# Kernel optimization log

Hardware: AMD Instinct MI355X
Metric: run time of the kernel (lower is better)

## Reference

```python
import jax, jax.numpy as jnp
import numpy as np
import math

B, T, C, H = 4, 2048, 1024, 16
D = C // H  # head dim = 64


def setup_inputs() -> dict:
    key = jax.random.key(0)
    ks = jax.random.split(key, 5)
    scale = 0.02
    x = jax.random.normal(ks[0], (B, T, C), dtype=jnp.float32)
    # torch nn.Linear(n_embd, 3*n_embd): weight [3C, C]; we store transposed [C, 3C]
    W_kqv = jax.random.normal(ks[1], (C, 3 * C), dtype=jnp.float32) * scale
    b_kqv = jnp.zeros((3 * C,), dtype=jnp.float32)
    W_proj = jax.random.normal(ks[2], (C, C), dtype=jnp.float32) * scale
    b_proj = jnp.zeros((C,), dtype=jnp.float32)
    padding_mask = jnp.ones((B, T), dtype=jnp.int32)  # 1 = valid token
    return {"x": x, "W_kqv": W_kqv, "b_kqv": b_kqv, "W_proj": W_proj,
            "b_proj": b_proj, "padding_mask": padding_mask}


def reference(x, W_kqv, b_kqv, W_proj, b_proj, padding_mask):
    Bx, Tx, Cx = x.shape
    kqv = x @ W_kqv + b_kqv                      # [B,T,3C]
    # original splits as k, q, v (in that order)
    k, q, v = jnp.split(kqv, 3, axis=2)
    def heads(t):
        return t.reshape(Bx, Tx, H, D).transpose(0, 2, 1, 3)  # [B,H,T,D]
    k, q, v = heads(k), heads(q), heads(v)
    att = jnp.einsum('bhqd,bhkd->bhqk', q, k) * (1.0 / math.sqrt(D))  # [B,H,T,T]
    causal = jnp.tril(jnp.ones((Tx, Tx), dtype=bool))[None, None]     # [1,1,T,T]
    valid = causal & (padding_mask[:, None, None, :] != 0)            # [B,1,T,T] broadcast
    neg_inf = jnp.finfo(att.dtype).min
    att = jnp.where(valid, att, neg_inf)
    att = jax.nn.softmax(att, axis=-1)
    y = jnp.einsum('bhqk,bhkd->bhqd', att, v)    # [B,H,T,D]
    y = y.transpose(0, 2, 1, 3).reshape(Bx, Tx, Cx)
    return y @ W_proj + b_proj
```

## Files before the change

### kernel.cpp

```cpp
#include <hip/hip_runtime.h>


typedef short bf16x8 __attribute__((ext_vector_type(8)));
typedef float floatx4 __attribute__((ext_vector_type(4)));

#define MFMA16(a, b, c) __builtin_amdgcn_mfma_f32_16x16x32_bf16(a, b, c, 0, 0, 0)

#define ASYNC_COPY16(gp, lp)                                                   \
  __builtin_amdgcn_global_load_lds(                                            \
      (__attribute__((address_space(1))) void*)(gp),                           \
      (__attribute__((address_space(3))) void*)(lp), 16, 0, 0)

#define DRAIN_VMCNT() asm volatile("s_waitcnt vmcnt(0)" ::: "memory")

#if defined(__has_builtin)
#if __has_builtin(__builtin_amdgcn_exp2f)
#define EXP2(x) __builtin_amdgcn_exp2f(x)
#endif
#endif
#ifndef EXP2
#define EXP2(x) exp2f(x)
#endif

__device__ __forceinline__ short f2bf(float f) {
  union { float f; unsigned u; } c;
  c.f = f;
  unsigned r = c.u + 0x7fffu + ((c.u >> 16) & 1u);
  return (short)(r >> 16);
}

__global__ __launch_bounds__(256) void cvt_f32_bf16(const float* __restrict__ in,
                                                    short* __restrict__ out) {
  int i = (blockIdx.x * 256 + threadIdx.x) * 4;
  float4 v = *(const float4*)&in[i];
  short4 o;
  o.x = f2bf(v.x); o.y = f2bf(v.y); o.z = f2bf(v.z); o.w = f2bf(v.w);
  *(short4*)&out[i] = o;
}

__global__ __launch_bounds__(256) void pmb_kernel(const int* __restrict__ pm,
                                                  float* __restrict__ pmbf) {
  int i = blockIdx.x * 256 + threadIdx.x;
  pmbf[i] = pm[i] ? 0.0f : -3.0e38f;
}

__global__ __launch_bounds__(256) void transpose_cvt_tiled(const float* __restrict__ in,
                                                           short* __restrict__ out,
                                                           int N) {
  __shared__ float buf[64][65];
  const int t = threadIdx.x;
  const int k0 = blockIdx.y * 64, n0 = blockIdx.x * 64;
#pragma unroll
  for (int i = 0; i < 4; ++i) {
    int s = t + i * 256;
    int row = s >> 4, c4 = (s & 15) * 4;
    float4 v = *(const float4*)&in[(size_t)(k0 + row) * N + n0 + c4];
    buf[row][c4] = v.x; buf[row][c4 + 1] = v.y;
    buf[row][c4 + 2] = v.z; buf[row][c4 + 3] = v.w;
  }
  __syncthreads();
#pragma unroll
  for (int i = 0; i < 2; ++i) {
    int u = t + i * 256;
    int rn = u >> 3, ch = (u & 7) * 8;
    short tmp[8];
#pragma unroll
    for (int j = 0; j < 8; ++j) tmp[j] = f2bf(buf[ch + j][rn]);
    *(uint4*)&out[(size_t)(n0 + rn) * 1024 + k0 + ch] = *(uint4*)tmp;
  }
}

template <int MODE>
__global__ __launch_bounds__(256) void gemm_bt128(const short* __restrict__ A,
                                                  const short* __restrict__ Bt,
                                                  const float* __restrict__ bias,
                                                  void* __restrict__ Cout,
                                                  int M, int N, int K) {
  __shared__ short smem[128 * 136];
  short* As = smem;
  short* Bs = smem + 8192;
  const int tid = threadIdx.x;
  const int lane = tid & 63;
  const int wv = tid >> 6;
  const int l15 = lane & 15, quad = lane >> 4;
  const int xr = l15 & 7;
  const int m0 = blockIdx.y * 128, n0 = blockIdx.x * 128;
  const int wm = (wv >> 1) * 64, wn = (wv & 1) * 64;

  floatx4 acc[4][4] = {};

  const int srow = tid >> 3;
  const int gch = ((tid & 7) ^ (srow & 7)) * 8;

  const short* Ap = &A[(size_t)(m0 + srow) * K + gch];
  const short* Bp = &Bt[(size_t)(n0 + srow) * K + gch];
  short* Asp = &As[tid * 8];
  short* Bsp = &Bs[tid * 8];

  for (int k0 = 0; k0 < K; k0 += 64) {
#pragma unroll
    for (int i = 0; i < 4; ++i) {
      ASYNC_COPY16(Ap + (size_t)(i * 32) * K + k0, Asp + i * 2048);
      ASYNC_COPY16(Bp + (size_t)(i * 32) * K + k0, Bsp + i * 2048);
    }
    DRAIN_VMCNT();
    __syncthreads();
#pragma unroll
    for (int s = 0; s < 2; ++s) {
      const int chs = ((s * 4 + quad) ^ xr) * 8;
      bf16x8 af[4], bfr[4];
#pragma unroll
      for (int i = 0; i < 4; ++i) {
        af[i]  = *(const bf16x8*)&As[(wm + i * 16 + l15) * 64 + chs];
        bfr[i] = *(const bf16x8*)&Bs[(wn + i * 16 + l15) * 64 + chs];
      }
#pragma unroll
      for (int mi = 0; mi < 4; ++mi)
#pragma unroll
        for (int ni = 0; ni < 4; ++ni)
          acc[mi][ni] = MFMA16(af[mi], bfr[ni], acc[mi][ni]);
    }
    __syncthreads();
  }

  if (MODE == 0) {
    float* outf = (float*)Cout;
#pragma unroll
    for (int ni = 0; ni < 4; ++ni) {
      int col = n0 + wn + ni * 16 + l15;
      float bv = bias[col];
#pragma unroll
      for (int mi = 0; mi < 4; ++mi) {
#pragma unroll
        for (int rr = 0; rr < 4; ++rr) {
          int row = m0 + wm + mi * 16 + quad * 4 + rr;
          outf[(size_t)row * N + col] = acc[mi][ni][rr] + bv;
        }
      }
    }
  } else {
    short* outs = (short*)Cout;
    const size_t QOFF = (size_t)64 * 2048 * 64;
    const int sec = n0 >> 10;
#pragma unroll
    for (int ni = 0; ni < 4; ++ni) {
      int c = wn + ni * 16 + l15;
      float bv = bias[n0 + c];
#pragma unroll
      for (int mi = 0; mi < 4; ++mi) {
        int r0 = wm + mi * 16 + quad * 4;
#pragma unroll
        for (int rr = 0; rr < 4; ++rr) {
          short v = f2bf(acc[mi][ni][rr] + bv);
          if (sec < 2) smem[(r0 + rr) * 136 + c] = v;
          else         smem[c * 136 + (r0 + rr)] = v;
        }
      }
    }
    __syncthreads();
#pragma unroll
    for (int j = 0; j < 8; ++j) {
      int idx = j * 256 + tid;
      int rr2 = idx >> 4;
      int cc2 = (idx & 15) * 8;
      uint4 v = *(const uint4*)&smem[rr2 * 136 + cc2];
      if (sec < 2) {
        int colg = n0 + cc2;
        int hh = (colg >> 6) & 15, dd = colg & 63;
        int row = m0 + rr2, bb = row >> 11, tt = row & 2047;
        *(uint4*)(outs + (size_t)sec * QOFF +
                  (((size_t)(bb * 16 + hh) * 2048 + tt) * 64 + dd)) = v;
      } else {
        int colg = n0 + rr2;
        int hh = (colg >> 6) & 15, dd = colg & 63;
        int row = m0 + cc2, bb = row >> 11, tt = row & 2047;
        *(uint4*)(outs + 2 * QOFF +
                  ((size_t)(bb * 16 + hh) * 64 + dd) * 2048 + tt) = v;
      }
    }
  }
}

__global__ __launch_bounds__(256, 3) void attn_flash8(const short* __restrict__ Qd,
                                                      const short* __restrict__ Kd,
                                                      const short* __restrict__ Vd,
                                                      const float* __restrict__ pmbf,
                                                      short* __restrict__ y) {
  constexpr int T = 2048, C = 1024;
  __shared__ short Ks[2][64 * 64];
  __shared__ short Vs[2][64 * 64];
  __shared__ short Ps[4][32][64];

  const int tid = threadIdx.x;
  const int lane = tid & 63, w = tid >> 6;
  const int l15 = lane & 15, quad = lane >> 4;
  const int xr = l15 & 7;
  const int lin = blockIdx.x;
  const int qb = 15 - (lin >> 6);
  const int bh = lin & 63;
  const int b = bh >> 4, h = bh & 15;
  const short* Qb = Qd + (size_t)bh * T * 64;
  const short* Kb = Kd + (size_t)bh * T * 64;
  const short* Vb = Vd + (size_t)bh * 64 * T;
  const float* pmb = &pmbf[b * T];
  const int q0 = qb * 128;
  const int nt = (q0 >> 6) + 2;

  const float SCALE2 = 0.18033688011112042f;

#define STAGE_KV(t, buf)                                                       \
  {                                                                            \
    const short* ksrc_ = Kb + (size_t)((t) * 64) * 64;                         \
    const short* vsrc_ = Vb + (t) * 64;                                        \
    _Pragma("unroll")                                                          \
    for (int j_ = 0; j_ < 2; ++j_) {                                           \
      int c_ = j_ * 256 + tid;                                                 \
      int r_ = c_ >> 3, cc_ = (c_ & 7) ^ (r_ & 7);                             \
      ASYNC_COPY16(ksrc_ + r_ * 64 + cc_ * 8, &Ks[buf][c_ * 8]);               \
      ASYNC_COPY16(vsrc_ + (size_t)r_ * T + cc_ * 8, &Vs[buf][c_ * 8]);        \
    }                                                                          \
  }

  bf16x8 qf[2][2];
#pragma unroll
  for (int mi = 0; mi < 2; ++mi) {
    const short* qp = Qb + (size_t)(q0 + w * 32 + mi * 16 + l15) * 64;
    qf[mi][0] = *(const bf16x8*)&qp[quad * 8];
    qf[mi][1] = *(const bf16x8*)&qp[32 + quad * 8];
  }

  floatx4 Oacc[2][4] = {};
  float lpart[2] = {};

  STAGE_KV(0, 0);
  DRAIN_VMCNT();
  __syncthreads();

  int cur = 0;
#pragma unroll 1
  for (int t = 0; t < nt; ++t) {
    const int k0 = t * 64;
    if (t + 1 < nt) STAGE_KV(t + 1, cur ^ 1);

    floatx4 Sacc[2][4] = {};
#pragma unroll
    for (int s = 0; s < 2; ++s) {
#pragma unroll
      for (int n4 = 0; n4 < 4; ++n4) {
        bf16x8 bK = *(const bf16x8*)
            &Ks[cur][(n4 * 16 + l15) * 64 + (((s * 4 + quad) ^ xr) * 8)];
        Sacc[0][n4] = MFMA16(bK, qf[0][s], Sacc[0][n4]);
        Sacc[1][n4] = MFMA16(bK, qf[1][s], Sacc[1][n4]);
      }
    }

    if (k0 < q0) {
#pragma unroll
      for (int n4 = 0; n4 < 4; ++n4) {
        floatx4 pb4 = *(const floatx4*)&pmb[k0 + n4 * 16 + quad * 4];
#pragma unroll
        for (int mi = 0; mi < 2; ++mi) {
          float p[4];
#pragma unroll
          for (int rr = 0; rr < 4; ++rr) {
            p[rr] = EXP2(fmaf(Sacc[mi][n4][rr], SCALE2, pb4[rr]));
            lpart[mi] += p[rr];
          }
          unsigned lo, hi;
          asm("v_cvt_pk_bf16_f32 %0, %1, %2" : "=v"(lo) : "v"(p[0]), "v"(p[1]));
          asm("v_cvt_pk_bf16_f32 %0, %1, %2" : "=v"(hi) : "v"(p[2]), "v"(p[3]));
          uint2 pk; pk.x = lo; pk.y = hi;
          *(uint2*)&Ps[w][mi * 16 + l15]
                      [((n4 * 2 + (quad >> 1)) ^ xr) * 8 + (quad & 1) * 4] = pk;
        }
      }
    } else {
#pragma unroll
      for (int n4 = 0; n4 < 4; ++n4) {
        floatx4 pb4 = *(const floatx4*)&pmb[k0 + n4 * 16 + quad * 4];
        const int colb = n4 * 16 + quad * 4;
#pragma unroll
        for (int mi = 0; mi < 2; ++mi) {
          const int rowb = (q0 - k0) + w * 32 + mi * 16 + l15;
          float p[4];
#pragma unroll
          for (int rr = 0; rr < 4; ++rr) {
            float v = EXP2(fmaf(Sacc[mi][n4][rr], SCALE2, pb4[rr]));
            if (colb + rr > rowb) v = 0.f;
            p[rr] = v;
            lpart[mi] += v;
          }
          unsigned lo, hi;
          asm("v_cvt_pk_bf16_f32 %0, %1, %2" : "=v"(lo) : "v"(p[0]), "v"(p[1]));
          asm("v_cvt_pk_bf16_f32 %0, %1, %2" : "=v"(hi) : "v"(p[2]), "v"(p[3]));
          uint2 pk; pk.x = lo; pk.y = hi;
          *(uint2*)&Ps[w][mi * 16 + l15]
                      [((n4 * 2 + (quad >> 1)) ^ xr) * 8 + (quad & 1) * 4] = pk;
        }
      }
    }

#pragma unroll
    for (int ks2 = 0; ks2 < 2; ++ks2) {
      const int pco = (((ks2 * 4 + quad) ^ xr) * 8);
      bf16x8 ap0 = *(const bf16x8*)&Ps[w][l15][pco];
      bf16x8 ap1 = *(const bf16x8*)&Ps[w][16 + l15][pco];
#pragma unroll
      for (int nd = 0; nd < 4; ++nd) {
        bf16x8 bV = *(const bf16x8*)
            &Vs[cur][(nd * 16 + l15) * 64 + (((ks2 * 4 + quad) ^ xr) * 8)];
        Oacc[0][nd] = MFMA16(ap0, bV, Oacc[0][nd]);
        Oacc[1][nd] = MFMA16(ap1, bV, Oacc[1][nd]);
      }
    }

    DRAIN_VMCNT();
    __syncthreads();
    cur ^= 1;
  }
#undef STAGE_KV

#pragma unroll
  for (int mi = 0; mi < 2; ++mi) {
    float s = lpart[mi];
    s += __shfl_xor(s, 16, 64);
    s += __shfl_xor(s, 32, 64);
    float inv_l[4];
#pragma unroll
    for (int rr = 0; rr < 4; ++rr)
      inv_l[rr] = 1.0f / __shfl(s, quad * 4 + rr, 16);
#pragma unroll
    for (int n = 0; n < 4; ++n) {
      int dcol = n * 16 + l15;
#pragma unroll
      for (int rr = 0; rr < 4; ++rr) {
        int rowq = q0 + w * 32 + mi * 16 + quad * 4 + rr;
        y[((size_t)(b * T + rowq)) * C + h * 64 + dcol] =
            f2bf(Oacc[mi][n][rr] * inv_l[rr]);
      }
    }
  }
}

extern "C" void kernel_launch(void* const* d_in, const int* in_sizes, int n_in,
                              void* d_out, int out_size, void* d_ws, size_t ws_size,
                              hipStream_t stream) {
  constexpr int B = 4, T = 2048, C = 1024;
  constexpr int M = B * T;
  constexpr int N1 = 3 * C;

  const float* x      = (const float*)d_in[0];
  const float* W_kqv  = (const float*)d_in[1];
  const float* b_kqv  = (const float*)d_in[2];
  const float* W_proj = (const float*)d_in[3];
  const float* b_proj = (const float*)d_in[4];
  const int*   pmask  = (const int*)d_in[5];
  float* out = (float*)d_out;

  const size_t QOFF = (size_t)64 * T * 64;

  short* xb     = (short*)d_ws;
  short* Wkqvt  = xb + (size_t)M * C;
  short* Wprojt = Wkqvt + (size_t)N1 * C;
  short* qkv    = Wprojt + (size_t)C * C;
  float* pmbf   = (float*)(qkv + 3 * QOFF);
  short* yb     = xb;

  short* Kd = qkv;
  short* Qd = qkv + QOFF;
  short* Vd = qkv + 2 * QOFF;

  cvt_f32_bf16<<<(M * C) / (256 * 4), 256, 0, stream>>>(x, xb);
  transpose_cvt_tiled<<<dim3(N1 / 64, 16), 256, 0, stream>>>(W_kqv, Wkqvt, N1);
  transpose_cvt_tiled<<<dim3(C / 64, 16), 256, 0, stream>>>(W_proj, Wprojt, C);
  pmb_kernel<<<(B * T) / 256, 256, 0, stream>>>(pmask, pmbf);

  gemm_bt128<2><<<dim3(N1 / 128, M / 128), 256, 0, stream>>>(xb, Wkqvt, b_kqv, Kd, M, N1, C);

  attn_flash8<<<dim3(1024), 256, 0, stream>>>(Qd, Kd, Vd, pmbf, yb);

  gemm_bt128<0><<<dim3(C / 128, M / 128), 256, 0, stream>>>(yb, Wprojt, b_proj, out, M, C, C);
}
```

Baseline: 254.6 us.

## Replace GEMM with 128x256 triple-buffered pipelined kernel using 512 threads

Replaces the 128x128 single-stage GEMM with a 128x256 tile kernel of 8 waves that triple-buffers A/B tiles in LDS. Async global-to-LDS loads for tile k+2 are split across two MFMA phases and waited with a partial vmcnt, so memory traffic overlaps compute. The kernel also raises wave priority around the MFMA blocks and uses XOR-swizzled epilogue staging to cut LDS bank conflicts. The cost is 144KB of LDS per block, which limits occupancy. The output projection launch also drops to 256 blocks, which may underfill the GPU.

```diff
diff --git a/kernel.cpp b/kernel.cpp
--- a/kernel.cpp
+++ b/kernel.cpp
@@ -12,6 +12,7 @@
       (__attribute__((address_space(3))) void*)(lp), 16, 0, 0)
 
 #define DRAIN_VMCNT() asm volatile("s_waitcnt vmcnt(0)" ::: "memory")
+#define WAIT_VMCNT6() asm volatile("s_waitcnt vmcnt(6)" ::: "memory")
 
 #if defined(__has_builtin)
 #if __has_builtin(__builtin_amdgcn_exp2f)
@@ -71,57 +72,96 @@
 }
 
 template <int MODE>
-__global__ __launch_bounds__(256) void gemm_bt128(const short* __restrict__ A,
-                                                  const short* __restrict__ Bt,
-                                                  const float* __restrict__ bias,
-                                                  void* __restrict__ Cout,
-                                                  int M, int N, int K) {
-  __shared__ short smem[128 * 136];
-  short* As = smem;
-  short* Bs = smem + 8192;
+__global__ __launch_bounds__(512, 2) void gemm_ph256(const short* __restrict__ A,
+                                                     const short* __restrict__ Bt,
+                                                     const float* __restrict__ bias,
+                                                     void* __restrict__ Cout,
+                                                     int M, int N, int K) {
+  __shared__ short smem[73728];
   const int tid = threadIdx.x;
   const int lane = tid & 63;
   const int wv = tid >> 6;
   const int l15 = lane & 15, quad = lane >> 4;
   const int xr = l15 & 7;
-  const int m0 = blockIdx.y * 128, n0 = blockIdx.x * 128;
-  const int wm = (wv >> 1) * 64, wn = (wv & 1) * 64;
+  const int m0 = blockIdx.y * 128, n0 = blockIdx.x * 256;
+  const int wm = (wv >> 2) * 64, wn = (wv & 3) * 64;
+  const int NT = K >> 6;
 
   floatx4 acc[4][4] = {};
 
-  const int srow = tid >> 3;
-  const int gch = ((tid & 7) ^ (srow & 7)) * 8;
-
-  const short* Ap = &A[(size_t)(m0 + srow) * K + gch];
-  const short* Bp = &Bt[(size_t)(n0 + srow) * K + gch];
-  short* Asp = &As[tid * 8];
-  short* Bsp = &Bs[tid * 8];
-
-  for (int k0 = 0; k0 < K; k0 += 64) {
-#pragma unroll
-    for (int i = 0; i < 4; ++i) {
-      ASYNC_COPY16(Ap + (size_t)(i * 32) * K + k0, Asp + i * 2048);
-      ASYNC_COPY16(Bp + (size_t)(i * 32) * K + k0, Bsp + i * 2048);
-    }
-    DRAIN_VMCNT();
-    __syncthreads();
-#pragma unroll
-    for (int s = 0; s < 2; ++s) {
-      const int chs = ((s * 4 + quad) ^ xr) * 8;
-      bf16x8 af[4], bfr[4];
-#pragma unroll
-      for (int i = 0; i < 4; ++i) {
-        af[i]  = *(const bf16x8*)&As[(wm + i * 16 + l15) * 64 + chs];
-        bfr[i] = *(const bf16x8*)&Bs[(wn + i * 16 + l15) * 64 + chs];
-      }
+#define STAGE_A(kt, bs, j)                                                     \
+  { int c_ = (j) * 512 + tid;                                                  \
+    int r_ = c_ >> 3, ch_ = (c_ & 7) ^ (r_ & 7);                               \
+    ASYNC_COPY16(&A[(size_t)(m0 + r_) * K + (kt) * 64 + ch_ * 8],              \
+                 &smem[(bs) * 8192 + c_ * 8]); }
+#define STAGE_B(kt, bs, j)                                                     \
+  { int c_ = (j) * 512 + tid;                                                  \
+    int r_ = c_ >> 3, ch_ = (c_ & 7) ^ (r_ & 7);                               \
+    ASYNC_COPY16(&Bt[(size_t)(n0 + r_) * K + (kt) * 64 + ch_ * 8],             \
+                 &smem[24576 + (bs) * 16384 + c_ * 8]); }
+
+  STAGE_A(0, 0, 0); STAGE_A(0, 0, 1);
+  STAGE_B(0, 0, 0); STAGE_B(0, 0, 1); STAGE_B(0, 0, 2); STAGE_B(0, 0, 3);
+  STAGE_A(1, 1, 0); STAGE_A(1, 1, 1);
+  STAGE_B(1, 1, 0); STAGE_B(1, 1, 1); STAGE_B(1, 1, 2); STAGE_B(1, 1, 3);
+  WAIT_VMCNT6();
+  __builtin_amdgcn_s_barrier();
+
+  int cur = 0, nxt = 2;
+  for (int kt = 0; kt < NT; ++kt) {
+    const bool st = (kt + 2 < NT);
+    const short* Asr = &smem[cur * 8192];
+    const short* Bsr = &smem[24576 + cur * 16384];
+
+    if (st) { STAGE_A(kt + 2, nxt, 0); STAGE_A(kt + 2, nxt, 1); STAGE_B(kt + 2, nxt, 0); }
+    bf16x8 af[4][2], bf0[2][2];
+#pragma unroll
+    for (int mi = 0; mi < 4; ++mi)
+#pragma unroll
+      for (int s = 0; s < 2; ++s)
+        af[mi][s] = *(const bf16x8*)
+            &Asr[(wm + mi * 16 + l15) * 64 + (((s * 4 + quad) ^ xr) * 8)];
+#pragma unroll
+    for (int nj = 0; nj < 2; ++nj)
+#pragma unroll
+      for (int s = 0; s < 2; ++s)
+        bf0[nj][s] = *(const bf16x8*)
+            &Bsr[(wn + nj * 16 + l15) * 64 + (((s * 4 + quad) ^ xr) * 8)];
+    __builtin_amdgcn_s_setprio(1);
+#pragma unroll
+    for (int s = 0; s < 2; ++s)
 #pragma unroll
       for (int mi = 0; mi < 4; ++mi)
 #pragma unroll
-        for (int ni = 0; ni < 4; ++ni)
-          acc[mi][ni] = MFMA16(af[mi], bfr[ni], acc[mi][ni]);
-    }
-    __syncthreads();
-  }
+        for (int nj = 0; nj < 2; ++nj)
+          acc[mi][nj] = MFMA16(af[mi][s], bf0[nj][s], acc[mi][nj]);
+    __builtin_amdgcn_s_setprio(0);
+    __builtin_amdgcn_s_barrier();
+
+    if (st) { STAGE_B(kt + 2, nxt, 1); STAGE_B(kt + 2, nxt, 2); STAGE_B(kt + 2, nxt, 3); }
+    bf16x8 bf1[2][2];
+#pragma unroll
+    for (int nj = 0; nj < 2; ++nj)
+#pragma unroll
+      for (int s = 0; s < 2; ++s)
+        bf1[nj][s] = *(const bf16x8*)
+            &Bsr[(wn + (2 + nj) * 16 + l15) * 64 + (((s * 4 + quad) ^ xr) * 8)];
+    __builtin_amdgcn_s_setprio(1);
+#pragma unroll
+    for (int s = 0; s < 2; ++s)
+#pragma unroll
+      for (int mi = 0; mi < 4; ++mi)
+#pragma unroll
+        for (int nj = 0; nj < 2; ++nj)
+          acc[mi][2 + nj] = MFMA16(af[mi][s], bf1[nj][s], acc[mi][2 + nj]);
+    __builtin_amdgcn_s_setprio(0);
+    if (st) { WAIT_VMCNT6(); } else { DRAIN_VMCNT(); }
+    __builtin_amdgcn_s_barrier();
+    cur = (cur == 2) ? 0 : cur + 1;
+    nxt = (nxt == 2) ? 0 : nxt + 1;
+  }
+#undef STAGE_A
+#undef STAGE_B
 
   if (MODE == 0) {
     float* outf = (float*)Cout;
@@ -142,38 +182,62 @@
     short* outs = (short*)Cout;
     const size_t QOFF = (size_t)64 * 2048 * 64;
     const int sec = n0 >> 10;
-#pragma unroll
-    for (int ni = 0; ni < 4; ++ni) {
-      int c = wn + ni * 16 + l15;
-      float bv = bias[n0 + c];
-#pragma unroll
-      for (int mi = 0; mi < 4; ++mi) {
-        int r0 = wm + mi * 16 + quad * 4;
-#pragma unroll
-        for (int rr = 0; rr < 4; ++rr) {
-          short v = f2bf(acc[mi][ni][rr] + bv);
-          if (sec < 2) smem[(r0 + rr) * 136 + c] = v;
-          else         smem[c * 136 + (r0 + rr)] = v;
+    short* Es = smem;
+    if (sec < 2) {
+#pragma unroll
+      for (int ni = 0; ni < 4; ++ni) {
+        int c = wn + ni * 16 + l15;
+        float bv = bias[n0 + c];
+#pragma unroll
+        for (int mi = 0; mi < 4; ++mi) {
+          int r0 = wm + mi * 16 + quad * 4;
+#pragma unroll
+          for (int rr = 0; rr < 4; ++rr) {
+            int r = r0 + rr;
+            Es[r * 256 + (c ^ (((r >> 2) & 3) << 4))] = f2bf(acc[mi][ni][rr] + bv);
+          }
         }
       }
+    } else {
+#pragma unroll
+      for (int ni = 0; ni < 4; ++ni) {
+        int c = wn + ni * 16 + l15;
+        float bv = bias[n0 + c];
+#pragma unroll
+        for (int mi = 0; mi < 4; ++mi) {
+          int r0 = wm + mi * 16 + quad * 4;
+#pragma unroll
+          for (int rr = 0; rr < 4; ++rr) {
+            int r = r0 + rr;
+            Es[c * 128 + (r ^ ((c & 7) << 3))] = f2bf(acc[mi][ni][rr] + bv);
+          }
+        }
+      }
     }
     __syncthreads();
-#pragma unroll
-    for (int j = 0; j < 8; ++j) {
-      int idx = j * 256 + tid;
-      int rr2 = idx >> 4;
-      int cc2 = (idx & 15) * 8;
-      uint4 v = *(const uint4*)&smem[rr2 * 136 + cc2];
-      if (sec < 2) {
+    if (sec < 2) {
+#pragma unroll
+      for (int jj = 0; jj < 8; ++jj) {
+        int idx = jj * 512 + tid;
+        int rr2 = idx >> 5;
+        int cc2 = (idx & 31) * 8;
+        uint4 v = *(const uint4*)&Es[rr2 * 256 + (cc2 ^ (((rr2 >> 2) & 3) << 4))];
         int colg = n0 + cc2;
         int hh = (colg >> 6) & 15, dd = colg & 63;
         int row = m0 + rr2, bb = row >> 11, tt = row & 2047;
         *(uint4*)(outs + (size_t)sec * QOFF +
                   (((size_t)(bb * 16 + hh) * 2048 + tt) * 64 + dd)) = v;
-      } else {
-        int colg = n0 + rr2;
+      }
+    } else {
+#pragma unroll
+      for (int jj = 0; jj < 8; ++jj) {
+        int idx = jj * 512 + tid;
+        int cd = idx >> 4;
+        int rb = (idx & 15) * 8;
+        uint4 v = *(const uint4*)&Es[cd * 128 + (rb ^ ((cd & 7) << 3))];
+        int colg = n0 + cd;
         int hh = (colg >> 6) & 15, dd = colg & 63;
-        int row = m0 + cc2, bb = row >> 11, tt = row & 2047;
+        int trow = m0 + rb, bb = trow >> 11, tt = trow & 2047;
         *(uint4*)(outs + 2 * QOFF +
                   ((size_t)(bb * 16 + hh) * 64 + dd) * 2048 + tt) = v;
       }
@@ -375,9 +439,9 @@
   transpose_cvt_tiled<<<dim3(C / 64, 16), 256, 0, stream>>>(W_proj, Wprojt, C);
   pmb_kernel<<<(B * T) / 256, 256, 0, stream>>>(pmask, pmbf);
 
-  gemm_bt128<2><<<dim3(N1 / 128, M / 128), 256, 0, stream>>>(xb, Wkqvt, b_kqv, Kd, M, N1, C);
+  gemm_ph256<2><<<dim3(N1 / 256, M / 128), 512, 0, stream>>>(xb, Wkqvt, b_kqv, Kd, M, N1, C);
 
   attn_flash8<<<dim3(1024), 256, 0, stream>>>(Qd, Kd, Vd, pmbf, yb);
 
-  gemm_bt128<0><<<dim3(C / 128, M / 128), 256, 0, stream>>>(yb, Wprojt, b_proj, out, M, C, C);
-}
+  gemm_ph256<0><<<dim3(C / 256, M / 128), 512, 0, stream>>>(yb, Wprojt, b_proj, out, M, C, C);
+}
```

New measurement: 252.6 us. About the same (-0.8%).
